# Performance work log

Measured on AMD Instinct MI355X. Metric: run time of the kernel, lower is better.

Reference implementation:

```python
import jax, jax.numpy as jnp
import numpy as np

B, S, D, H, DH, N, L, VOCAB = 8, 512, 1024, 16, 64, 32, 2, 128

def _ln(x, g, b, eps=1e-5):
    m = jnp.mean(x, axis=-1, keepdims=True)
    v = jnp.var(x, axis=-1, keepdims=True)
    return (x - m) * jax.lax.rsqrt(v + eps) * g + b

def setup_inputs() -> dict:
    key = jax.random.key(0)
    ks = jax.random.split(key, 10)
    std = 0.02
    inp = {
        "tokens": jax.random.randint(ks[0], (B, S), 0, VOCAB),
        "emb": jax.random.normal(ks[1], (VOCAB, D), jnp.float32) * std,
        "pos": jax.random.normal(ks[2], (1, S, D), jnp.float32) * std,
        "ln_g": jnp.ones((L, D), jnp.float32),
        "ln_b": jnp.zeros((L, D), jnp.float32),
        "wq": jax.random.normal(ks[3], (L, D, D), jnp.float32) * std,
        "bq": jnp.zeros((L, D), jnp.float32),
        "wk": jax.random.normal(ks[4], (L, D, D), jnp.float32) * std,
        "bk": jnp.zeros((L, D), jnp.float32),
        "wv": jax.random.normal(ks[5], (L, D, D), jnp.float32) * std,
        "bv": jnp.zeros((L, D), jnp.float32),
        "wg": jax.random.normal(ks[6], (L, D, D), jnp.float32) * std,
        "bg": jnp.zeros((L, D), jnp.float32),
        "wo": jax.random.normal(ks[7], (L, D, D), jnp.float32) * std,
        "bo": jnp.zeros((L, D), jnp.float32),
        "alpha_logit": jax.random.normal(ks[8], (L, H, N), jnp.float32) * 0.1,
        "fn_g": jnp.ones((D,), jnp.float32),
        "fn_b": jnp.zeros((D,), jnp.float32),
        "head_w": jax.random.normal(ks[9], (VOCAB, D), jnp.float32) * std,
        "head_b": jnp.zeros((VOCAB,), jnp.float32),
    }
    return inp

def _layer(x, g, b, Wq, Bq, Wk, Bk, Wv, Bv, Wg, Bg, Wo, Bo, alogit):
    residual = x
    xn = _ln(x, g, b)  # (B,S,D)
    def proj(W, Bb):
        return (jnp.einsum('bsd,ed->bse', xn, W) + Bb).reshape(x.shape[0], x.shape[1], H, DH)
    Q, K, V = proj(Wq, Bq), proj(Wk, Bk), proj(Wv, Bv)
    gate = jax.nn.silu(proj(Wg, Bg))
    alpha = jax.nn.sigmoid(alogit)  # (H,N)
    # scan over time; carry h: (B,H,N,DH)
    h0 = jnp.zeros((x.shape[0], H, N, DH), x.dtype)
    qkv = (jnp.moveaxis(Q, 1, 0), jnp.moveaxis(K, 1, 0), jnp.moveaxis(V, 1, 0))  # (S,B,H,DH)
    def step(h, qkv_t):
        q_t, k_t, v_t = qkv_t
        k_state = k_t[:, :, :N]  # state_dim <= d_head
        h = alpha[None, :, :, None] * h + jnp.einsum('bhi,bhj->bhij', k_state, v_t)
        q_state = q_t[:, :, :N]
        o_t = jnp.einsum('bhi,bhij->bhj', q_state, h)
        return h, o_t
    _, O = jax.lax.scan(step, h0, qkv)  # O: (S,B,H,DH)
    o = jnp.moveaxis(O, 0, 1) * gate  # (B,S,H,DH)
    o = o.reshape(x.shape[0], x.shape[1], H * DH)
    y = jnp.einsum('bsd,ed->bse', o, Wo) + Bo
    return residual + y

def reference(tokens, emb, pos, ln_g, ln_b, wq, bq, wk, bk, wv, bv, wg, bg, wo, bo,
              alpha_logit, fn_g, fn_b, head_w, head_b):
    x = emb[tokens] + pos[:, :tokens.shape[1], :]
    for l in range(L):
        x = _layer(x, ln_g[l], ln_b[l], wq[l], bq[l], wk[l], bk[l], wv[l], bv[l],
                   wg[l], bg[l], wo[l], bo[l], alpha_logit[l])
    x = _ln(x, fn_g, fn_b)
    logits = jnp.einsum('bsd,vd->bsv', x, head_w) + head_b
    return logits
```

## Files before the change

### kernel.cpp

```cpp
#include <hip/hip_runtime.h>
#include <hip/hip_bf16.h>
#include <stdint.h>

#define D_MODEL 1024
#define BB 8
#define SS 512
#define HH 16
#define DHH 64
#define NN 32
#define LL 2
#define VOC 128
#define M_TOK (BB * SS)
#define CHUNK 32
#define NCHUNK 16
#define PRO 16

typedef __bf16 bf16x8_t __attribute__((ext_vector_type(8)));
typedef float floatx4_t __attribute__((ext_vector_type(4)));
typedef unsigned short u16;
typedef unsigned short u16x8 __attribute__((ext_vector_type(8)));

__device__ __forceinline__ float b2f(u16 u) {
  union { unsigned int i; float f; } c; c.i = ((unsigned int)u) << 16; return c.f;
}
__device__ __forceinline__ u16 f2b(float f) {
  union { float f; unsigned int i; } c; c.f = f;
  unsigned int r = c.i + 0x7fffu + ((c.i >> 16) & 1u);
  return (u16)(r >> 16);
}
__device__ __forceinline__ float sigm(float x) {
  return 1.0f / (1.0f + __expf(-x));
}

#define WSEG 524288
#define HSEG 32768
#define TOT4 (5 * WSEG + HSEG)
struct SrcP { const float* p[6]; };

__global__ __launch_bounds__(256) void k_pre(
    SrcP src, u16* __restrict__ dst,
    const int* __restrict__ tok, const float* __restrict__ emb,
    const float* __restrict__ pos, const float* __restrict__ g,
    const float* __restrict__ b, float* __restrict__ x, u16* __restrict__ xn) {
  int bid = blockIdx.x;
  int t = threadIdx.x;
  if (bid < 1024) {
    int wv = t >> 6, lane = t & 63;
    int m = bid * 4 + wv;
    int s = m & (SS - 1);
    int tkn = tok[m];
    const float4* er = (const float4*)(emb + (size_t)tkn * D_MODEL);
    const float4* pr = (const float4*)(pos + (size_t)s * D_MODEL);
    float4* xr = (float4*)(x + (size_t)m * D_MODEL);
    float4 v[4];
    float s1 = 0.f, s2 = 0.f;
#pragma unroll
    for (int c = 0; c < 4; ++c) {
      int f4 = c * 64 + lane;
      float4 e = er[f4], p = pr[f4];
      v[c].x = e.x + p.x; v[c].y = e.y + p.y;
      v[c].z = e.z + p.z; v[c].w = e.w + p.w;
      xr[f4] = v[c];
      s1 += v[c].x + v[c].y + v[c].z + v[c].w;
      s2 += v[c].x * v[c].x + v[c].y * v[c].y + v[c].z * v[c].z + v[c].w * v[c].w;
    }
#pragma unroll
    for (int o = 1; o < 64; o <<= 1) {
      s1 += __shfl_xor(s1, o);
      s2 += __shfl_xor(s2, o);
    }
    float mean = s1 * (1.0f / D_MODEL);
    float var = s2 * (1.0f / D_MODEL) - mean * mean;
    float rstd = rsqrtf(var + 1e-5f);
    ushort4* xo = (ushort4*)(xn + (size_t)m * D_MODEL);
#pragma unroll
    for (int c = 0; c < 4; ++c) {
      int f4 = c * 64 + lane;
      float4 gv = ((const float4*)g)[f4];
      float4 bv = ((const float4*)b)[f4];
      ushort4 ov;
      ov.x = f2b((v[c].x - mean) * rstd * gv.x + bv.x);
      ov.y = f2b((v[c].y - mean) * rstd * gv.y + bv.y);
      ov.z = f2b((v[c].z - mean) * rstd * gv.z + bv.z);
      ov.w = f2b((v[c].w - mean) * rstd * gv.w + bv.w);
      xo[f4] = ov;
    }
  } else {
    for (int i = (bid - 1024) * 256 + t; i < TOT4; i += 1024 * 256) {
      int seg, within;
      if (i < 5 * WSEG) { seg = i / WSEG; within = i - seg * WSEG; }
      else { seg = 5; within = i - 5 * WSEG; }
      float4 v = ((const float4*)src.p[seg])[within];
      ushort4 o;
      o.x = f2b(v.x); o.y = f2b(v.y); o.z = f2b(v.z); o.w = f2b(v.w);
      ((ushort4*)dst)[(size_t)seg * WSEG + within] = o;
    }
  }
}

__global__ __launch_bounds__(256) void k_ln(
    const float* __restrict__ x, const float* __restrict__ g,
    const float* __restrict__ b, u16* __restrict__ xn) {
  int t = threadIdx.x;
  int wv = t >> 6, lane = t & 63;
  int m = blockIdx.x * 4 + wv;
  const float4* xr = (const float4*)(x + (size_t)m * D_MODEL);
  float4 v[4];
  float s1 = 0.f, s2 = 0.f;
#pragma unroll
  for (int c = 0; c < 4; ++c) {
    int f4 = c * 64 + lane;
    v[c] = xr[f4];
    s1 += v[c].x + v[c].y + v[c].z + v[c].w;
    s2 += v[c].x * v[c].x + v[c].y * v[c].y + v[c].z * v[c].z + v[c].w * v[c].w;
  }
#pragma unroll
  for (int o = 1; o < 64; o <<= 1) {
    s1 += __shfl_xor(s1, o);
    s2 += __shfl_xor(s2, o);
  }
  float mean = s1 * (1.0f / D_MODEL);
  float var = s2 * (1.0f / D_MODEL) - mean * mean;
  float rstd = rsqrtf(var + 1e-5f);
  ushort4* xo = (ushort4*)(xn + (size_t)m * D_MODEL);
#pragma unroll
  for (int c = 0; c < 4; ++c) {
    int f4 = c * 64 + lane;
    float4 gv = ((const float4*)g)[f4];
    float4 bv = ((const float4*)b)[f4];
    ushort4 ov;
    ov.x = f2b((v[c].x - mean) * rstd * gv.x + bv.x);
    ov.y = f2b((v[c].y - mean) * rstd * gv.y + bv.y);
    ov.z = f2b((v[c].z - mean) * rstd * gv.z + bv.z);
    ov.w = f2b((v[c].w - mean) * rstd * gv.w + bv.w);
    xo[f4] = ov;
  }
}

__global__ __launch_bounds__(256) void k_head_red(
    const u16* __restrict__ Ph, const float* __restrict__ hb,
    float* __restrict__ out) {
  int i4 = blockIdx.x * 256 + threadIdx.x;
  float4 s = ((const float4*)hb)[i4 & 31];
#pragma unroll
  for (int z = 0; z < 8; ++z) {
    ushort4 p = *(const ushort4*)&Ph[(size_t)z * M_TOK * VOC + (size_t)i4 * 4];
    s.x += b2f(p.x); s.y += b2f(p.y); s.z += b2f(p.z); s.w += b2f(p.w);
  }
  ((float4*)out)[i4] = s;
}

struct Task { const u16* W; const float* bias; void* out; };
struct Tasks { Task t[4]; };

__device__ __forceinline__ void async_cp16(const void* g, void* l) {
  __builtin_amdgcn_global_load_lds(
      (const __attribute__((address_space(1))) void*)g,
      (__attribute__((address_space(3))) void*)l, 16, 0, 0);
}

template <int EPI>
__global__ __launch_bounds__(256) void k_gemm(
    const u16* __restrict__ A, Tasks tasks, int N, int K, int kspan,
    size_t pstride) {
  __shared__ u16 ldsA[128 * 64];
  __shared__ u16 ldsB[128 * 64];
  const int tid = threadIdx.x;
  const int lane = tid & 63, wv = tid >> 6;
  const int bm = blockIdx.x * 128, bn = blockIdx.y * 128;
  const Task tk = tasks.t[EPI == 5 ? 0 : blockIdx.z];
  const u16* W = tk.W;
  const int kb = (EPI == 5) ? blockIdx.z * kspan : 0;
  const int ke = kb + kspan;

  const int wm = (wv >> 1) * 64, wn = (wv & 1) * 64;
  floatx4_t acc[4][4];
#pragma unroll
  for (int i = 0; i < 4; ++i)
#pragma unroll
    for (int j = 0; j < 4; ++j)
#pragma unroll
      for (int r = 0; r < 4; ++r) acc[i][j][r] = 0.0f;

  const int srow = lane >> 3;
  const int sk8 = (lane & 7) ^ srow;

  for (int k0 = kb; k0 < ke; k0 += 64) {
#pragma unroll
    for (int c = 0; c < 4; ++c) {
      int chunk = wv * 4 + c;
      const u16* ga = A + (size_t)(bm + chunk * 8 + srow) * K + (k0 + sk8 * 8);
      async_cp16(ga, &ldsA[chunk * 512]);
      const u16* gb = W + (size_t)(bn + chunk * 8 + srow) * K + (k0 + sk8 * 8);
      async_cp16(gb, &ldsB[chunk * 512]);
    }
    __syncthreads();
#pragma unroll
    for (int kt = 0; kt < 2; ++kt) {
      const int k8 = kt * 4 + (lane >> 4);
      bf16x8_t af[4], bfr[4];
#pragma unroll
      for (int mi = 0; mi < 4; ++mi) {
        int row = wm + mi * 16 + (lane & 15);
        int gran = row * 8 + (k8 ^ (row & 7));
        af[mi] = *(const bf16x8_t*)&ldsA[gran * 8];
      }
#pragma unroll
      for (int ni = 0; ni < 4; ++ni) {
        int row = wn + ni * 16 + (lane & 15);
        int gran = row * 8 + (k8 ^ (row & 7));
        bfr[ni] = *(const bf16x8_t*)&ldsB[gran * 8];
      }
#pragma unroll
      for (int mi = 0; mi < 4; ++mi)
#pragma unroll
        for (int ni = 0; ni < 4; ++ni)
          acc[mi][ni] = __builtin_amdgcn_mfma_f32_16x16x32_bf16(
              af[mi], bfr[ni], acc[mi][ni], 0, 0, 0);
    }
    __syncthreads();
  }

  u16* outp16 = (EPI == 5)
      ? (u16*)tk.out + (size_t)blockIdx.z * pstride : (u16*)tk.out;
#pragma unroll
  for (int ni = 0; ni < 4; ++ni) {
    int col = bn + wn + ni * 16 + (lane & 15);
    float bias = (EPI == 2) ? tk.bias[col] : 0.0f;
#pragma unroll
    for (int mi = 0; mi < 4; ++mi) {
      int row0 = bm + wm + mi * 16 + (lane >> 4) * 4;
#pragma unroll
      for (int r = 0; r < 4; ++r) {
        size_t idx = (size_t)(row0 + r) * N + col;
        outp16[idx] = f2b(acc[mi][ni][r] + bias);
      }
    }
  }
}

__global__ __launch_bounds__(256) void k_gemm_wo(
    const u16* __restrict__ A, const u16* __restrict__ W,
    const float* __restrict__ bias, float* __restrict__ x) {
  __shared__ u16 ldsA[64 * 64];
  __shared__ u16 ldsB[128 * 64];
  const int tid = threadIdx.x;
  const int lane = tid & 63, wv = tid >> 6;
  const int bm = blockIdx.x * 64, bn = blockIdx.y * 128;
  const int K = D_MODEL;

  const int wm = (wv >> 1) * 32, wn = (wv & 1) * 64;
  floatx4_t acc[2][4];
#pragma unroll
  for (int i = 0; i < 2; ++i)
#pragma unroll
    for (int j = 0; j < 4; ++j)
#pragma unroll
      for (int r = 0; r < 4; ++r) acc[i][j][r] = 0.0f;

  const int srow = lane >> 3;
  const int sk8 = (lane & 7) ^ srow;

  for (int k0 = 0; k0 < K; k0 += 64) {
#pragma unroll
    for (int c = 0; c < 2; ++c) {
      int chunk = wv * 2 + c;
      const u16* ga = A + (size_t)(bm + chunk * 8 + srow) * K + (k0 + sk8 * 8);
      async_cp16(ga, &ldsA[chunk * 512]);
    }
#pragma unroll
    for (int c = 0; c < 4; ++c) {
      int chunk = wv * 4 + c;
      const u16* gb = W + (size_t)(bn + chunk * 8 + srow) * K + (k0 + sk8 * 8);
      async_cp16(gb, &ldsB[chunk * 512]);
    }
    __syncthreads();
#pragma unroll
    for (int kt = 0; kt < 2; ++kt) {
      const int k8 = kt * 4 + (lane >> 4);
      bf16x8_t af[2], bfr[4];
#pragma unroll
      for (int mi = 0; mi < 2; ++mi) {
        int row = wm + mi * 16 + (lane & 15);
        int gran = row * 8 + (k8 ^ (row & 7));
        af[mi] = *(const bf16x8_t*)&ldsA[gran * 8];
      }
#pragma unroll
      for (int ni = 0; ni < 4; ++ni) {
        int row = wn + ni * 16 + (lane & 15);
        int gran = row * 8 + (k8 ^ (row & 7));
        bfr[ni] = *(const bf16x8_t*)&ldsB[gran * 8];
      }
#pragma unroll
      for (int mi = 0; mi < 2; ++mi)
#pragma unroll
        for (int ni = 0; ni < 4; ++ni)
          acc[mi][ni] = __builtin_amdgcn_mfma_f32_16x16x32_bf16(
              af[mi], bfr[ni], acc[mi][ni], 0, 0, 0);
    }
    __syncthreads();
  }

#pragma unroll
  for (int ni = 0; ni < 4; ++ni) {
    int col = bn + wn + ni * 16 + (lane & 15);
    float bb = bias[col];
#pragma unroll
    for (int mi = 0; mi < 2; ++mi) {
      int row0 = bm + wm + mi * 16 + (lane >> 4) * 4;
#pragma unroll
      for (int r = 0; r < 4; ++r) {
        size_t idx = (size_t)(row0 + r) * D_MODEL + col;
        x[idx] += acc[mi][ni][r] + bb;
      }
    }
  }
}

__global__ __launch_bounds__(128) void k_scan_f(
    const u16* __restrict__ Q, const u16* __restrict__ K,
    const u16* __restrict__ V, const u16* __restrict__ G,
    const float* __restrict__ alog, u16* __restrict__ og) {
  int blk = blockIdx.x;
  int bh = blk >> 4;
  int c = blk & (NCHUNK - 1);
  int b = bh >> 4, h = bh & 15;
  int t = threadIdx.x;
  int jl = t & 31, ig = t >> 5;
  int i0 = ig * 8, j0 = jl * 2;

  __shared__ u16 kp[PRO][32];
  __shared__ u16 vp[PRO][64];
  __shared__ u16 ql[CHUNK][32];
  __shared__ u16 kl[CHUNK][32];
  __shared__ u16 vl[CHUNK][64];
  __shared__ u16 gl[CHUNK][64];
  __shared__ float po[2][CHUNK][64];

  size_t base = (size_t)b * SS * 1024 + h * 64 + (size_t)c * CHUNK * 1024;
  size_t basep = base - (size_t)PRO * 1024;
  {
    int s = t >> 2, e = (t & 3) * 8;
    *(u16x8*)&ql[s][e] = *(const u16x8*)&Q[base + (size_t)s * 1024 + e];
    *(u16x8*)&kl[s][e] = *(const u16x8*)&K[base + (size_t)s * 1024 + e];
    if (c > 0 && t < 64)
      *(u16x8*)&kp[s][e] = *(const u16x8*)&K[basep + (size_t)s * 1024 + e];
  }
#pragma unroll
  for (int r = 0; r < 2; ++r) {
    int idx = t + r * 128;
    int s = idx >> 3, e = (idx & 7) * 8;
    *(u16x8*)&vl[s][e] = *(const u16x8*)&V[base + (size_t)s * 1024 + e];
    *(u16x8*)&gl[s][e] = *(const u16x8*)&G[base + (size_t)s * 1024 + e];
  }
  if (c > 0) {
    int s = t >> 3, e = (t & 7) * 8;
    *(u16x8*)&vp[s][e] = *(const u16x8*)&V[basep + (size_t)s * 1024 + e];
  }
  __syncthreads();

  float al[8];
#pragma unroll
  for (int u = 0; u < 8; ++u) al[u] = sigm(alog[h * NN + i0 + u]);

  float hr[8][2];
#pragma unroll
  for (int u = 0; u < 8; ++u) { hr[u][0] = 0.f; hr[u][1] = 0.f; }

  if (c > 0) {
    for (int s = 0; s < PRO; ++s) {
      ushort4 kA = *(const ushort4*)&kp[s][i0];
      ushort4 kB = *(const ushort4*)&kp[s][i0 + 4];
      float kc[8] = {b2f(kA.x), b2f(kA.y), b2f(kA.z), b2f(kA.w),
                     b2f(kB.x), b2f(kB.y), b2f(kB.z), b2f(kB.w)};
      float vx = b2f(vp[s][j0]), vy = b2f(vp[s][j0 + 1]);
#pragma unroll
      for (int u = 0; u < 8; ++u) {
        hr[u][0] = al[u] * hr[u][0] + kc[u] * vx;
        hr[u][1] = al[u] * hr[u][1] + kc[u] * vy;
      }
    }
  }

  for (int s = 0; s < CHUNK; ++s) {
    ushort4 kA = *(const ushort4*)&kl[s][i0];
    ushort4 kB = *(const ushort4*)&kl[s][i0 + 4];
    ushort4 qA = *(const ushort4*)&ql[s][i0];
    ushort4 qB = *(const ushort4*)&ql[s][i0 + 4];
    float kc[8] = {b2f(kA.x), b2f(kA.y), b2f(kA.z), b2f(kA.w),
                   b2f(kB.x), b2f(kB.y), b2f(kB.z), b2f(kB.w)};
    float qc[8] = {b2f(qA.x), b2f(qA.y), b2f(qA.z), b2f(qA.w),
                   b2f(qB.x), b2f(qB.y), b2f(qB.z), b2f(qB.w)};
    float vx = b2f(vl[s][j0]), vy = b2f(vl[s][j0 + 1]);
    float p0 = 0.f, p1 = 0.f;
#pragma unroll
    for (int u = 0; u < 8; ++u) {
      float h0 = al[u] * hr[u][0] + kc[u] * vx;
      float h1 = al[u] * hr[u][1] + kc[u] * vy;
      hr[u][0] = h0; hr[u][1] = h1;
      p0 += qc[u] * h0;
      p1 += qc[u] * h1;
    }
    p0 += __shfl_xor(p0, 32);
    p1 += __shfl_xor(p1, 32);
    if (!(t & 32)) *(float2*)&po[t >> 6][s][j0] = make_float2(p0, p1);
  }
  __syncthreads();

#pragma unroll
  for (int r = 0; r < 8; ++r) {
    int idx = t + r * 128;
    int s = idx >> 5, jp = (idx & 31) * 2;
    float o0 = po[0][s][jp] + po[1][s][jp];
    float o1 = po[0][s][jp + 1] + po[1][s][jp + 1];
    float g0 = b2f(gl[s][jp]), g1 = b2f(gl[s][jp + 1]);
    ushort2 st;
    st.x = f2b(o0 * g0 * sigm(g0));
    st.y = f2b(o1 * g1 * sigm(g1));
    *(ushort2*)&og[((size_t)b * SS + c * CHUNK + s) * 1024 + h * 64 + jp] = st;
  }
}

extern "C" void kernel_launch(void* const* d_in, const int* in_sizes, int n_in,
                              void* d_out, int out_size, void* d_ws, size_t ws_size,
                              hipStream_t stream) {
  const int*   tok  = (const int*)d_in[0];
  const float* emb  = (const float*)d_in[1];
  const float* pos  = (const float*)d_in[2];
  const float* ln_g = (const float*)d_in[3];
  const float* ln_b = (const float*)d_in[4];
  const float* wq   = (const float*)d_in[5];
  const float* bq   = (const float*)d_in[6];
  const float* wk   = (const float*)d_in[7];
  const float* bk   = (const float*)d_in[8];
  const float* wv   = (const float*)d_in[9];
  const float* bv   = (const float*)d_in[10];
  const float* wg   = (const float*)d_in[11];
  const float* bg   = (const float*)d_in[12];
  const float* wo   = (const float*)d_in[13];
  const float* bo   = (const float*)d_in[14];
  const float* alog = (const float*)d_in[15];
  const float* fn_g = (const float*)d_in[16];
  const float* fn_b = (const float*)d_in[17];
  const float* hw   = (const float*)d_in[18];
  const float* hb   = (const float*)d_in[19];

  char* ws = (char*)d_ws;
  float* x   = (float*)(ws);
  u16*   xn  = (u16*)(ws + (size_t)(16 << 20));
  u16*   qb  = (u16*)(ws + (size_t)(24 << 20));
  u16*   kb  = (u16*)(ws + (size_t)(32 << 20));
  u16*   vb  = (u16*)(ws + (size_t)(40 << 20));
  u16*   gb  = (u16*)(ws + (size_t)(48 << 20));
  u16*   Ph  = (u16*)(ws + (size_t)(56 << 20));
  u16*   wB  = (u16*)(ws + (size_t)(72 << 20));
  u16* wqB = wB;
  u16* wkB = wB + (size_t)2 * 1024 * 1024;
  u16* wvB = wB + (size_t)4 * 1024 * 1024;
  u16* wgB = wB + (size_t)6 * 1024 * 1024;
  u16* woB = wB + (size_t)8 * 1024 * 1024;
  u16* hwB = wB + (size_t)10 * 1024 * 1024;

  SrcP sp; sp.p[0] = wq; sp.p[1] = wk; sp.p[2] = wv; sp.p[3] = wg; sp.p[4] = wo; sp.p[5] = hw;
  k_pre<<<2048, 256, 0, stream>>>(sp, wB, tok, emb, pos, ln_g, ln_b, x, xn);

  for (int l = 0; l < LL; ++l) {
    Tasks tq;
    tq.t[0] = Task{wqB + (size_t)l * D_MODEL * D_MODEL, bq + l * D_MODEL, (void*)qb};
    tq.t[1] = Task{wkB + (size_t)l * D_MODEL * D_MODEL, bk + l * D_MODEL, (void*)kb};
    tq.t[2] = Task{wvB + (size_t)l * D_MODEL * D_MODEL, bv + l * D_MODEL, (void*)vb};
    tq.t[3] = Task{wgB + (size_t)l * D_MODEL * D_MODEL, bg + l * D_MODEL, (void*)gb};
    k_gemm<2><<<dim3(32, 8, 4), 256, 0, stream>>>(xn, tq, D_MODEL, D_MODEL,
                                                  D_MODEL, 0);

    k_scan_f<<<128 * NCHUNK, 128, 0, stream>>>(
        qb, kb, vb, gb, alog + l * HH * NN, xn);

    k_gemm_wo<<<dim3(64, 8), 256, 0, stream>>>(
        xn, woB + (size_t)l * D_MODEL * D_MODEL, bo + l * D_MODEL, x);

    const float* ng = (l + 1 < LL) ? ln_g + (l + 1) * D_MODEL : fn_g;
    const float* nb = (l + 1 < LL) ? ln_b + (l + 1) * D_MODEL : fn_b;
    k_ln<<<1024, 256, 0, stream>>>(x, ng, nb, xn);
  }

  Tasks th;
  th.t[0] = Task{hwB, hb, (void*)Ph};
  th.t[1] = th.t[0]; th.t[2] = th.t[0]; th.t[3] = th.t[0];
  k_gemm<5><<<dim3(32, 1, 8), 256, 0, stream>>>(xn, th, VOC, D_MODEL,
                                                128, (size_t)M_TOK * VOC);
  k_head_red<<<512, 256, 0, stream>>>(Ph, hb, (float*)d_out);
}
```

Before: 344.7 us.

## Fuse whole forward pass into one persistent megakernel with grid barriers

Replaces the chain of separate launches (preprocess, QKVG GEMM, chunked scan, Wo GEMM, layernorm, head GEMM and reduction) with a single persistent kernel. It loops over virtual blocks and synchronises phases with a software grid barrier built on atomics. The scan chunk size is halved and the scan work is re-split into 256-thread units using a union of LDS buffers. This removes launch gaps and tail effects between stages, at the cost of global barrier overhead, reduced occupancy from the launch bounds, and a deadlock risk if the chosen grid cannot be fully co-resident.

```diff
diff --git a/kernel.cpp b/kernel.cpp
--- a/kernel.cpp
+++ b/kernel.cpp
@@ -11,8 +11,8 @@
 #define LL 2
 #define VOC 128
 #define M_TOK (BB * SS)
-#define CHUNK 32
-#define NCHUNK 16
+#define CHUNK 16
+#define NCHUNK 32
 #define PRO 16
 
 typedef __bf16 bf16x8_t __attribute__((ext_vector_type(8)));
@@ -37,80 +37,282 @@
 #define TOT4 (5 * WSEG + HSEG)
 struct SrcP { const float* p[6]; };
 
-__global__ __launch_bounds__(256) void k_pre(
-    SrcP src, u16* __restrict__ dst,
-    const int* __restrict__ tok, const float* __restrict__ emb,
-    const float* __restrict__ pos, const float* __restrict__ g,
-    const float* __restrict__ b, float* __restrict__ x, u16* __restrict__ xn) {
-  int bid = blockIdx.x;
-  int t = threadIdx.x;
-  if (bid < 1024) {
-    int wv = t >> 6, lane = t & 63;
-    int m = bid * 4 + wv;
-    int s = m & (SS - 1);
-    int tkn = tok[m];
-    const float4* er = (const float4*)(emb + (size_t)tkn * D_MODEL);
-    const float4* pr = (const float4*)(pos + (size_t)s * D_MODEL);
-    float4* xr = (float4*)(x + (size_t)m * D_MODEL);
-    float4 v[4];
-    float s1 = 0.f, s2 = 0.f;
+struct ScanU {
+  u16 ql[CHUNK][32]; u16 kl[CHUNK][32];
+  u16 vl[CHUNK][64]; u16 gl[CHUNK][64];
+  u16 kp[PRO][32];   u16 vp[PRO][64];
+  float po[CHUNK][64];
+};
+union LdsU {
+  struct { u16 A[128 * 64]; u16 B[128 * 64]; } g;
+  ScanU s[2];
+};
+
+__device__ __forceinline__ void async_cp16(const void* g, void* l) {
+  __builtin_amdgcn_global_load_lds(
+      (const __attribute__((address_space(1))) void*)g,
+      (__attribute__((address_space(3))) void*)l, 16, 0, 0);
+}
+
+__device__ void gbar(unsigned* cnt, unsigned* gen, unsigned& lg) {
+  __threadfence();
+  __syncthreads();
+  if (threadIdx.x == 0) {
+    unsigned g = lg;
+    if (atomicAdd(cnt, 1u) == gridDim.x - 1u) {
+      atomicExch(cnt, 0u);
+      __threadfence();
+      atomicAdd(gen, 1u);
+    } else {
+      while (atomicAdd(gen, 0u) == g) __builtin_amdgcn_s_sleep(8);
+    }
+    lg = g + 1u;
+  }
+  __syncthreads();
+  __threadfence();
+}
+
+__device__ void gemm128(const u16* __restrict__ A, const u16* __restrict__ W,
+                        const float* __restrict__ bias, u16* __restrict__ out,
+                        int N, int K, int kb, int ke, int bx, int by, int tid,
+                        u16* ldsA, u16* ldsB, bool addBias) {
+  const int lane = tid & 63, wv = tid >> 6;
+  const int bm = bx * 128, bn = by * 128;
+  const int wm = (wv >> 1) * 64, wn = (wv & 1) * 64;
+  floatx4_t acc[4][4];
+#pragma unroll
+  for (int i = 0; i < 4; ++i)
+#pragma unroll
+    for (int j = 0; j < 4; ++j)
+#pragma unroll
+      for (int r = 0; r < 4; ++r) acc[i][j][r] = 0.0f;
+
+  const int srow = lane >> 3;
+  const int sk8 = (lane & 7) ^ srow;
+
+  for (int k0 = kb; k0 < ke; k0 += 64) {
 #pragma unroll
     for (int c = 0; c < 4; ++c) {
-      int f4 = c * 64 + lane;
-      float4 e = er[f4], p = pr[f4];
-      v[c].x = e.x + p.x; v[c].y = e.y + p.y;
-      v[c].z = e.z + p.z; v[c].w = e.w + p.w;
-      xr[f4] = v[c];
-      s1 += v[c].x + v[c].y + v[c].z + v[c].w;
-      s2 += v[c].x * v[c].x + v[c].y * v[c].y + v[c].z * v[c].z + v[c].w * v[c].w;
-    }
-#pragma unroll
-    for (int o = 1; o < 64; o <<= 1) {
-      s1 += __shfl_xor(s1, o);
-      s2 += __shfl_xor(s2, o);
-    }
-    float mean = s1 * (1.0f / D_MODEL);
-    float var = s2 * (1.0f / D_MODEL) - mean * mean;
-    float rstd = rsqrtf(var + 1e-5f);
-    ushort4* xo = (ushort4*)(xn + (size_t)m * D_MODEL);
+      int chunk = wv * 4 + c;
+      const u16* ga = A + (size_t)(bm + chunk * 8 + srow) * K + (k0 + sk8 * 8);
+      async_cp16(ga, &ldsA[chunk * 512]);
+      const u16* gb = W + (size_t)(bn + chunk * 8 + srow) * K + (k0 + sk8 * 8);
+      async_cp16(gb, &ldsB[chunk * 512]);
+    }
+    __syncthreads();
+#pragma unroll
+    for (int kt = 0; kt < 2; ++kt) {
+      const int k8 = kt * 4 + (lane >> 4);
+      bf16x8_t af[4], bfr[4];
+#pragma unroll
+      for (int mi = 0; mi < 4; ++mi) {
+        int row = wm + mi * 16 + (lane & 15);
+        int gran = row * 8 + (k8 ^ (row & 7));
+        af[mi] = *(const bf16x8_t*)&ldsA[gran * 8];
+      }
+#pragma unroll
+      for (int ni = 0; ni < 4; ++ni) {
+        int row = wn + ni * 16 + (lane & 15);
+        int gran = row * 8 + (k8 ^ (row & 7));
+        bfr[ni] = *(const bf16x8_t*)&ldsB[gran * 8];
+      }
+#pragma unroll
+      for (int mi = 0; mi < 4; ++mi)
+#pragma unroll
+        for (int ni = 0; ni < 4; ++ni)
+          acc[mi][ni] = __builtin_amdgcn_mfma_f32_16x16x32_bf16(
+              af[mi], bfr[ni], acc[mi][ni], 0, 0, 0);
+    }
+    __syncthreads();
+  }
+
+#pragma unroll
+  for (int ni = 0; ni < 4; ++ni) {
+    int col = bn + wn + ni * 16 + (lane & 15);
+    float bb = addBias ? bias[col] : 0.0f;
+#pragma unroll
+    for (int mi = 0; mi < 4; ++mi) {
+      int row0 = bm + wm + mi * 16 + (lane >> 4) * 4;
+#pragma unroll
+      for (int r = 0; r < 4; ++r)
+        out[(size_t)(row0 + r) * N + col] = f2b(acc[mi][ni][r] + bb);
+    }
+  }
+}
+
+__device__ void wo64(const u16* __restrict__ A, const u16* __restrict__ W,
+                     const float* __restrict__ bias, float* __restrict__ x,
+                     int bx, int by, int tid, u16* ldsA, u16* ldsB) {
+  const int lane = tid & 63, wv = tid >> 6;
+  const int bm = bx * 64, bn = by * 128;
+  const int K = D_MODEL;
+  const int wm = (wv >> 1) * 32, wn = (wv & 1) * 64;
+  floatx4_t acc[2][4];
+#pragma unroll
+  for (int i = 0; i < 2; ++i)
+#pragma unroll
+    for (int j = 0; j < 4; ++j)
+#pragma unroll
+      for (int r = 0; r < 4; ++r) acc[i][j][r] = 0.0f;
+
+  const int srow = lane >> 3;
+  const int sk8 = (lane & 7) ^ srow;
+
+  for (int k0 = 0; k0 < K; k0 += 64) {
+#pragma unroll
+    for (int c = 0; c < 2; ++c) {
+      int chunk = wv * 2 + c;
+      const u16* ga = A + (size_t)(bm + chunk * 8 + srow) * K + (k0 + sk8 * 8);
+      async_cp16(ga, &ldsA[chunk * 512]);
+    }
 #pragma unroll
     for (int c = 0; c < 4; ++c) {
-      int f4 = c * 64 + lane;
-      float4 gv = ((const float4*)g)[f4];
-      float4 bv = ((const float4*)b)[f4];
-      ushort4 ov;
-      ov.x = f2b((v[c].x - mean) * rstd * gv.x + bv.x);
-      ov.y = f2b((v[c].y - mean) * rstd * gv.y + bv.y);
-      ov.z = f2b((v[c].z - mean) * rstd * gv.z + bv.z);
-      ov.w = f2b((v[c].w - mean) * rstd * gv.w + bv.w);
-      xo[f4] = ov;
-    }
-  } else {
-    for (int i = (bid - 1024) * 256 + t; i < TOT4; i += 1024 * 256) {
-      int seg, within;
-      if (i < 5 * WSEG) { seg = i / WSEG; within = i - seg * WSEG; }
-      else { seg = 5; within = i - 5 * WSEG; }
-      float4 v = ((const float4*)src.p[seg])[within];
-      ushort4 o;
-      o.x = f2b(v.x); o.y = f2b(v.y); o.z = f2b(v.z); o.w = f2b(v.w);
-      ((ushort4*)dst)[(size_t)seg * WSEG + within] = o;
-    }
-  }
-}
-
-__global__ __launch_bounds__(256) void k_ln(
-    const float* __restrict__ x, const float* __restrict__ g,
-    const float* __restrict__ b, u16* __restrict__ xn) {
-  int t = threadIdx.x;
+      int chunk = wv * 4 + c;
+      const u16* gb = W + (size_t)(bn + chunk * 8 + srow) * K + (k0 + sk8 * 8);
+      async_cp16(gb, &ldsB[chunk * 512]);
+    }
+    __syncthreads();
+#pragma unroll
+    for (int kt = 0; kt < 2; ++kt) {
+      const int k8 = kt * 4 + (lane >> 4);
+      bf16x8_t af[2], bfr[4];
+#pragma unroll
+      for (int mi = 0; mi < 2; ++mi) {
+        int row = wm + mi * 16 + (lane & 15);
+        int gran = row * 8 + (k8 ^ (row & 7));
+        af[mi] = *(const bf16x8_t*)&ldsA[gran * 8];
+      }
+#pragma unroll
+      for (int ni = 0; ni < 4; ++ni) {
+        int row = wn + ni * 16 + (lane & 15);
+        int gran = row * 8 + (k8 ^ (row & 7));
+        bfr[ni] = *(const bf16x8_t*)&ldsB[gran * 8];
+      }
+#pragma unroll
+      for (int mi = 0; mi < 2; ++mi)
+#pragma unroll
+        for (int ni = 0; ni < 4; ++ni)
+          acc[mi][ni] = __builtin_amdgcn_mfma_f32_16x16x32_bf16(
+              af[mi], bfr[ni], acc[mi][ni], 0, 0, 0);
+    }
+    __syncthreads();
+  }
+
+#pragma unroll
+  for (int ni = 0; ni < 4; ++ni) {
+    int col = bn + wn + ni * 16 + (lane & 15);
+    float bb = bias[col];
+#pragma unroll
+    for (int mi = 0; mi < 2; ++mi) {
+      int row0 = bm + wm + mi * 16 + (lane >> 4) * 4;
+#pragma unroll
+      for (int r = 0; r < 4; ++r)
+        x[(size_t)(row0 + r) * D_MODEL + col] += acc[mi][ni][r] + bb;
+    }
+  }
+}
+
+__device__ void scan_unit(ScanU* S, int vu, int tl,
+                          const u16* __restrict__ Q, const u16* __restrict__ K,
+                          const u16* __restrict__ V, const u16* __restrict__ G,
+                          const float* __restrict__ alog, u16* __restrict__ og) {
+  int bh = vu >> 5;
+  int c = vu & (NCHUNK - 1);
+  int b = bh >> 4, h = bh & 15;
+  int j = tl & 63, ig = tl >> 6, i0 = ig * 16;
+
+  size_t base = (size_t)b * SS * 1024 + h * 64 + (size_t)c * CHUNK * 1024;
+  size_t basep = base - (size_t)PRO * 1024;
+  {
+    int u6 = tl & 63;
+    int sq = u6 >> 2, e = (u6 & 3) * 8;
+    if (tl < 64)
+      *(u16x8*)&S->ql[sq][e] = *(const u16x8*)&Q[base + (size_t)sq * 1024 + e];
+    else
+      *(u16x8*)&S->kl[sq][e] = *(const u16x8*)&K[base + (size_t)sq * 1024 + e];
+    int sv = tl >> 3, ev = (tl & 7) * 8;
+    *(u16x8*)&S->vl[sv][ev] = *(const u16x8*)&V[base + (size_t)sv * 1024 + ev];
+    *(u16x8*)&S->gl[sv][ev] = *(const u16x8*)&G[base + (size_t)sv * 1024 + ev];
+    if (c > 0) {
+      if (tl < 64)
+        *(u16x8*)&S->kp[sq][e] = *(const u16x8*)&K[basep + (size_t)sq * 1024 + e];
+      *(u16x8*)&S->vp[sv][ev] = *(const u16x8*)&V[basep + (size_t)sv * 1024 + ev];
+    }
+  }
+  __syncthreads();
+
+  float al[16];
+#pragma unroll
+  for (int u = 0; u < 16; ++u) al[u] = sigm(alog[h * NN + i0 + u]);
+  float hr[16];
+#pragma unroll
+  for (int u = 0; u < 16; ++u) hr[u] = 0.f;
+
+  if (c > 0) {
+    for (int s = 0; s < PRO; ++s) {
+      u16x8 kA = *(const u16x8*)&S->kp[s][i0];
+      u16x8 kB = *(const u16x8*)&S->kp[s][i0 + 8];
+      float vx = b2f(S->vp[s][j]);
+#pragma unroll
+      for (int u = 0; u < 8; ++u) hr[u] = al[u] * hr[u] + b2f(kA[u]) * vx;
+#pragma unroll
+      for (int u = 0; u < 8; ++u) hr[8 + u] = al[8 + u] * hr[8 + u] + b2f(kB[u]) * vx;
+    }
+  }
+
+  float pr[16];
+#pragma unroll
+  for (int s = 0; s < CHUNK; ++s) {
+    u16x8 kA = *(const u16x8*)&S->kl[s][i0];
+    u16x8 kB = *(const u16x8*)&S->kl[s][i0 + 8];
+    u16x8 qA = *(const u16x8*)&S->ql[s][i0];
+    u16x8 qB = *(const u16x8*)&S->ql[s][i0 + 8];
+    float vx = b2f(S->vl[s][j]);
+    float p = 0.f;
+#pragma unroll
+    for (int u = 0; u < 8; ++u) {
+      hr[u] = al[u] * hr[u] + b2f(kA[u]) * vx;
+      p += b2f(qA[u]) * hr[u];
+    }
+#pragma unroll
+    for (int u = 0; u < 8; ++u) {
+      hr[8 + u] = al[8 + u] * hr[8 + u] + b2f(kB[u]) * vx;
+      p += b2f(qB[u]) * hr[8 + u];
+    }
+    if (ig) S->po[s][j] = p; else pr[s] = p;
+  }
+  __syncthreads();
+
+  if (ig == 0) {
+#pragma unroll
+    for (int s = 0; s < CHUNK; ++s) {
+      float o = pr[s] + S->po[s][j];
+      float gg = b2f(S->gl[s][j]);
+      og[((size_t)b * SS + c * CHUNK + s) * 1024 + h * 64 + j] =
+          f2b(o * gg * sigm(gg));
+    }
+  }
+}
+
+__device__ void embed_ln_dev(const int* tok, const float* emb, const float* pos,
+                             const float* g, const float* b, float* x, u16* xn,
+                             int blk, int t) {
   int wv = t >> 6, lane = t & 63;
-  int m = blockIdx.x * 4 + wv;
-  const float4* xr = (const float4*)(x + (size_t)m * D_MODEL);
+  int m = blk * 4 + wv;
+  int s = m & (SS - 1);
+  int tkn = tok[m];
+  const float4* er = (const float4*)(emb + (size_t)tkn * D_MODEL);
+  const float4* pr = (const float4*)(pos + (size_t)s * D_MODEL);
+  float4* xr = (float4*)(x + (size_t)m * D_MODEL);
   float4 v[4];
   float s1 = 0.f, s2 = 0.f;
 #pragma unroll
   for (int c = 0; c < 4; ++c) {
     int f4 = c * 64 + lane;
-    v[c] = xr[f4];
+    float4 e = er[f4], p = pr[f4];
+    v[c].x = e.x + p.x; v[c].y = e.y + p.y;
+    v[c].z = e.z + p.z; v[c].w = e.w + p.w;
+    xr[f4] = v[c];
     s1 += v[c].x + v[c].y + v[c].z + v[c].w;
     s2 += v[c].x * v[c].x + v[c].y * v[c].y + v[c].z * v[c].z + v[c].w * v[c].w;
   }
@@ -137,287 +339,133 @@
   }
 }
 
-__global__ __launch_bounds__(256) void k_head_red(
-    const u16* __restrict__ Ph, const float* __restrict__ hb,
-    float* __restrict__ out) {
-  int i4 = blockIdx.x * 256 + threadIdx.x;
-  float4 s = ((const float4*)hb)[i4 & 31];
-#pragma unroll
-  for (int z = 0; z < 8; ++z) {
-    ushort4 p = *(const ushort4*)&Ph[(size_t)z * M_TOK * VOC + (size_t)i4 * 4];
-    s.x += b2f(p.x); s.y += b2f(p.y); s.z += b2f(p.z); s.w += b2f(p.w);
-  }
-  ((float4*)out)[i4] = s;
-}
-
-struct Task { const u16* W; const float* bias; void* out; };
-struct Tasks { Task t[4]; };
-
-__device__ __forceinline__ void async_cp16(const void* g, void* l) {
-  __builtin_amdgcn_global_load_lds(
-      (const __attribute__((address_space(1))) void*)g,
-      (__attribute__((address_space(3))) void*)l, 16, 0, 0);
-}
-
-template <int EPI>
-__global__ __launch_bounds__(256) void k_gemm(
-    const u16* __restrict__ A, Tasks tasks, int N, int K, int kspan,
-    size_t pstride) {
-  __shared__ u16 ldsA[128 * 64];
-  __shared__ u16 ldsB[128 * 64];
-  const int tid = threadIdx.x;
-  const int lane = tid & 63, wv = tid >> 6;
-  const int bm = blockIdx.x * 128, bn = blockIdx.y * 128;
-  const Task tk = tasks.t[EPI == 5 ? 0 : blockIdx.z];
-  const u16* W = tk.W;
-  const int kb = (EPI == 5) ? blockIdx.z * kspan : 0;
-  const int ke = kb + kspan;
-
-  const int wm = (wv >> 1) * 64, wn = (wv & 1) * 64;
-  floatx4_t acc[4][4];
-#pragma unroll
-  for (int i = 0; i < 4; ++i)
-#pragma unroll
-    for (int j = 0; j < 4; ++j)
-#pragma unroll
-      for (int r = 0; r < 4; ++r) acc[i][j][r] = 0.0f;
-
-  const int srow = lane >> 3;
-  const int sk8 = (lane & 7) ^ srow;
-
-  for (int k0 = kb; k0 < ke; k0 += 64) {
-#pragma unroll
-    for (int c = 0; c < 4; ++c) {
-      int chunk = wv * 4 + c;
-      const u16* ga = A + (size_t)(bm + chunk * 8 + srow) * K + (k0 + sk8 * 8);
-      async_cp16(ga, &ldsA[chunk * 512]);
-      const u16* gb = W + (size_t)(bn + chunk * 8 + srow) * K + (k0 + sk8 * 8);
-      async_cp16(gb, &ldsB[chunk * 512]);
-    }
-    __syncthreads();
-#pragma unroll
-    for (int kt = 0; kt < 2; ++kt) {
-      const int k8 = kt * 4 + (lane >> 4);
-      bf16x8_t af[4], bfr[4];
-#pragma unroll
-      for (int mi = 0; mi < 4; ++mi) {
-        int row = wm + mi * 16 + (lane & 15);
-        int gran = row * 8 + (k8 ^ (row & 7));
-        af[mi] = *(const bf16x8_t*)&ldsA[gran * 8];
+__device__ void ln_dev(const float* x, const float* g, const float* b,
+                       u16* xn, int blk, int t) {
+  int wv = t >> 6, lane = t & 63;
+  int m = blk * 4 + wv;
+  const float4* xr = (const float4*)(x + (size_t)m * D_MODEL);
+  float4 v[4];
+  float s1 = 0.f, s2 = 0.f;
+#pragma unroll
+  for (int c = 0; c < 4; ++c) {
+    int f4 = c * 64 + lane;
+    v[c] = xr[f4];
+    s1 += v[c].x + v[c].y + v[c].z + v[c].w;
+    s2 += v[c].x * v[c].x + v[c].y * v[c].y + v[c].z * v[c].z + v[c].w * v[c].w;
+  }
+#pragma unroll
+  for (int o = 1; o < 64; o <<= 1) {
+    s1 += __shfl_xor(s1, o);
+    s2 += __shfl_xor(s2, o);
+  }
+  float mean = s1 * (1.0f / D_MODEL);
+  float var = s2 * (1.0f / D_MODEL) - mean * mean;
+  float rstd = rsqrtf(var + 1e-5f);
+  ushort4* xo = (ushort4*)(xn + (size_t)m * D_MODEL);
+#pragma unroll
+  for (int c = 0; c < 4; ++c) {
+    int f4 = c * 64 + lane;
+    float4 gv = ((const float4*)g)[f4];
+    float4 bv = ((const float4*)b)[f4];
+    ushort4 ov;
+    ov.x = f2b((v[c].x - mean) * rstd * gv.x + bv.x);
+    ov.y = f2b((v[c].y - mean) * rstd * gv.y + bv.y);
+    ov.z = f2b((v[c].z - mean) * rstd * gv.z + bv.z);
+    ov.w = f2b((v[c].w - mean) * rstd * gv.w + bv.w);
+    xo[f4] = ov;
+  }
+}
+
+struct MegaParams {
+  const int* tok; const float* emb; const float* pos;
+  const float* ln_g; const float* ln_b;
+  const float* bq; const float* bk; const float* bv; const float* bg;
+  const float* bo; const float* alog;
+  const float* fn_g; const float* fn_b; const float* hb;
+  SrcP src;
+  float* x; u16* xn; u16* qb; u16* kb; u16* vb; u16* gb; u16* Ph; u16* wB;
+  unsigned* bar;
+  float* out;
+};
+
+__global__ __launch_bounds__(256, 4) void k_mega(MegaParams P) {
+  __shared__ LdsU L;
+  const int blk = blockIdx.x;
+  const int G = gridDim.x;
+  const int t = threadIdx.x;
+  unsigned lg = 0;
+  unsigned* cnt = P.bar;
+  unsigned* gen = P.bar + 1;
+
+  for (int vb = blk; vb < 1024; vb += G)
+    embed_ln_dev(P.tok, P.emb, P.pos, P.ln_g, P.ln_b, P.x, P.xn, vb, t);
+  for (int i = blk * 256 + t; i < TOT4; i += G * 256) {
+    int seg, within;
+    if (i < 5 * WSEG) { seg = i / WSEG; within = i - seg * WSEG; }
+    else { seg = 5; within = i - 5 * WSEG; }
+    float4 v = ((const float4*)P.src.p[seg])[within];
+    ushort4 o;
+    o.x = f2b(v.x); o.y = f2b(v.y); o.z = f2b(v.z); o.w = f2b(v.w);
+    ((ushort4*)P.wB)[(size_t)seg * WSEG + within] = o;
+  }
+  gbar(cnt, gen, lg);
+
+  for (int l = 0; l < LL; ++l) {
+    for (int vb = blk; vb < 1024; vb += G) {
+      int bx = vb & 31, by = (vb >> 5) & 7, bz = vb >> 8;
+      const u16* Wt = P.wB + (size_t)bz * 2097152 + (size_t)l * 1048576;
+      const float* bias =
+          (bz == 0 ? P.bq : bz == 1 ? P.bk : bz == 2 ? P.bv : P.bg) + l * D_MODEL;
+      u16* out = bz == 0 ? P.qb : bz == 1 ? P.kb : bz == 2 ? P.vb : P.gb;
+      gemm128(P.xn, Wt, bias, out, D_MODEL, D_MODEL, 0, D_MODEL,
+              bx, by, t, L.g.A, L.g.B, true);
+    }
+    gbar(cnt, gen, lg);
+
+    {
+      const float* al = P.alog + l * HH * NN;
+      int unit = t >> 7, tl = t & 127;
+      int iters = 4096 / (2 * G);
+      for (int it = 0; it < iters; ++it) {
+        int vu = it * 2 * G + blk * 2 + unit;
+        scan_unit(&L.s[unit], vu, tl, P.qb, P.kb, P.vb, P.gb, al, P.xn);
+        __syncthreads();
       }
-#pragma unroll
-      for (int ni = 0; ni < 4; ++ni) {
-        int row = wn + ni * 16 + (lane & 15);
-        int gran = row * 8 + (k8 ^ (row & 7));
-        bfr[ni] = *(const bf16x8_t*)&ldsB[gran * 8];
-      }
-#pragma unroll
-      for (int mi = 0; mi < 4; ++mi)
-#pragma unroll
-        for (int ni = 0; ni < 4; ++ni)
-          acc[mi][ni] = __builtin_amdgcn_mfma_f32_16x16x32_bf16(
-              af[mi], bfr[ni], acc[mi][ni], 0, 0, 0);
-    }
-    __syncthreads();
-  }
-
-  u16* outp16 = (EPI == 5)
-      ? (u16*)tk.out + (size_t)blockIdx.z * pstride : (u16*)tk.out;
-#pragma unroll
-  for (int ni = 0; ni < 4; ++ni) {
-    int col = bn + wn + ni * 16 + (lane & 15);
-    float bias = (EPI == 2) ? tk.bias[col] : 0.0f;
-#pragma unroll
-    for (int mi = 0; mi < 4; ++mi) {
-      int row0 = bm + wm + mi * 16 + (lane >> 4) * 4;
-#pragma unroll
-      for (int r = 0; r < 4; ++r) {
-        size_t idx = (size_t)(row0 + r) * N + col;
-        outp16[idx] = f2b(acc[mi][ni][r] + bias);
-      }
-    }
-  }
-}
-
-__global__ __launch_bounds__(256) void k_gemm_wo(
-    const u16* __restrict__ A, const u16* __restrict__ W,
-    const float* __restrict__ bias, float* __restrict__ x) {
-  __shared__ u16 ldsA[64 * 64];
-  __shared__ u16 ldsB[128 * 64];
-  const int tid = threadIdx.x;
-  const int lane = tid & 63, wv = tid >> 6;
-  const int bm = blockIdx.x * 64, bn = blockIdx.y * 128;
-  const int K = D_MODEL;
-
-  const int wm = (wv >> 1) * 32, wn = (wv & 1) * 64;
-  floatx4_t acc[2][4];
-#pragma unroll
-  for (int i = 0; i < 2; ++i)
-#pragma unroll
-    for (int j = 0; j < 4; ++j)
-#pragma unroll
-      for (int r = 0; r < 4; ++r) acc[i][j][r] = 0.0f;
-
-  const int srow = lane >> 3;
-  const int sk8 = (lane & 7) ^ srow;
-
-  for (int k0 = 0; k0 < K; k0 += 64) {
-#pragma unroll
-    for (int c = 0; c < 2; ++c) {
-      int chunk = wv * 2 + c;
-      const u16* ga = A + (size_t)(bm + chunk * 8 + srow) * K + (k0 + sk8 * 8);
-      async_cp16(ga, &ldsA[chunk * 512]);
-    }
-#pragma unroll
-    for (int c = 0; c < 4; ++c) {
-      int chunk = wv * 4 + c;
-      const u16* gb = W + (size_t)(bn + chunk * 8 + srow) * K + (k0 + sk8 * 8);
-      async_cp16(gb, &ldsB[chunk * 512]);
-    }
-    __syncthreads();
-#pragma unroll
-    for (int kt = 0; kt < 2; ++kt) {
-      const int k8 = kt * 4 + (lane >> 4);
-      bf16x8_t af[2], bfr[4];
-#pragma unroll
-      for (int mi = 0; mi < 2; ++mi) {
-        int row = wm + mi * 16 + (lane & 15);
-        int gran = row * 8 + (k8 ^ (row & 7));
-        af[mi] = *(const bf16x8_t*)&ldsA[gran * 8];
-      }
-#pragma unroll
-      for (int ni = 0; ni < 4; ++ni) {
-        int row = wn + ni * 16 + (lane & 15);
-        int gran = row * 8 + (k8 ^ (row & 7));
-        bfr[ni] = *(const bf16x8_t*)&ldsB[gran * 8];
-      }
-#pragma unroll
-      for (int mi = 0; mi < 2; ++mi)
-#pragma unroll
-        for (int ni = 0; ni < 4; ++ni)
-          acc[mi][ni] = __builtin_amdgcn_mfma_f32_16x16x32_bf16(
-              af[mi], bfr[ni], acc[mi][ni], 0, 0, 0);
-    }
-    __syncthreads();
-  }
-
-#pragma unroll
-  for (int ni = 0; ni < 4; ++ni) {
-    int col = bn + wn + ni * 16 + (lane & 15);
-    float bb = bias[col];
-#pragma unroll
-    for (int mi = 0; mi < 2; ++mi) {
-      int row0 = bm + wm + mi * 16 + (lane >> 4) * 4;
-#pragma unroll
-      for (int r = 0; r < 4; ++r) {
-        size_t idx = (size_t)(row0 + r) * D_MODEL + col;
-        x[idx] += acc[mi][ni][r] + bb;
-      }
-    }
-  }
-}
-
-__global__ __launch_bounds__(128) void k_scan_f(
-    const u16* __restrict__ Q, const u16* __restrict__ K,
-    const u16* __restrict__ V, const u16* __restrict__ G,
-    const float* __restrict__ alog, u16* __restrict__ og) {
-  int blk = blockIdx.x;
-  int bh = blk >> 4;
-  int c = blk & (NCHUNK - 1);
-  int b = bh >> 4, h = bh & 15;
-  int t = threadIdx.x;
-  int jl = t & 31, ig = t >> 5;
-  int i0 = ig * 8, j0 = jl * 2;
-
-  __shared__ u16 kp[PRO][32];
-  __shared__ u16 vp[PRO][64];
-  __shared__ u16 ql[CHUNK][32];
-  __shared__ u16 kl[CHUNK][32];
-  __shared__ u16 vl[CHUNK][64];
-  __shared__ u16 gl[CHUNK][64];
-  __shared__ float po[2][CHUNK][64];
-
-  size_t base = (size_t)b * SS * 1024 + h * 64 + (size_t)c * CHUNK * 1024;
-  size_t basep = base - (size_t)PRO * 1024;
-  {
-    int s = t >> 2, e = (t & 3) * 8;
-    *(u16x8*)&ql[s][e] = *(const u16x8*)&Q[base + (size_t)s * 1024 + e];
-    *(u16x8*)&kl[s][e] = *(const u16x8*)&K[base + (size_t)s * 1024 + e];
-    if (c > 0 && t < 64)
-      *(u16x8*)&kp[s][e] = *(const u16x8*)&K[basep + (size_t)s * 1024 + e];
-  }
-#pragma unroll
-  for (int r = 0; r < 2; ++r) {
-    int idx = t + r * 128;
-    int s = idx >> 3, e = (idx & 7) * 8;
-    *(u16x8*)&vl[s][e] = *(const u16x8*)&V[base + (size_t)s * 1024 + e];
-    *(u16x8*)&gl[s][e] = *(const u16x8*)&G[base + (size_t)s * 1024 + e];
-  }
-  if (c > 0) {
-    int s = t >> 3, e = (t & 7) * 8;
-    *(u16x8*)&vp[s][e] = *(const u16x8*)&V[basep + (size_t)s * 1024 + e];
-  }
-  __syncthreads();
-
-  float al[8];
-#pragma unroll
-  for (int u = 0; u < 8; ++u) al[u] = sigm(alog[h * NN + i0 + u]);
-
-  float hr[8][2];
-#pragma unroll
-  for (int u = 0; u < 8; ++u) { hr[u][0] = 0.f; hr[u][1] = 0.f; }
-
-  if (c > 0) {
-    for (int s = 0; s < PRO; ++s) {
-      ushort4 kA = *(const ushort4*)&kp[s][i0];
-      ushort4 kB = *(const ushort4*)&kp[s][i0 + 4];
-      float kc[8] = {b2f(kA.x), b2f(kA.y), b2f(kA.z), b2f(kA.w),
-                     b2f(kB.x), b2f(kB.y), b2f(kB.z), b2f(kB.w)};
-      float vx = b2f(vp[s][j0]), vy = b2f(vp[s][j0 + 1]);
-#pragma unroll
-      for (int u = 0; u < 8; ++u) {
-        hr[u][0] = al[u] * hr[u][0] + kc[u] * vx;
-        hr[u][1] = al[u] * hr[u][1] + kc[u] * vy;
-      }
-    }
-  }
-
-  for (int s = 0; s < CHUNK; ++s) {
-    ushort4 kA = *(const ushort4*)&kl[s][i0];
-    ushort4 kB = *(const ushort4*)&kl[s][i0 + 4];
-    ushort4 qA = *(const ushort4*)&ql[s][i0];
-    ushort4 qB = *(const ushort4*)&ql[s][i0 + 4];
-    float kc[8] = {b2f(kA.x), b2f(kA.y), b2f(kA.z), b2f(kA.w),
-                   b2f(kB.x), b2f(kB.y), b2f(kB.z), b2f(kB.w)};
-    float qc[8] = {b2f(qA.x), b2f(qA.y), b2f(qA.z), b2f(qA.w),
-                   b2f(qB.x), b2f(qB.y), b2f(qB.z), b2f(qB.w)};
-    float vx = b2f(vl[s][j0]), vy = b2f(vl[s][j0 + 1]);
-    float p0 = 0.f, p1 = 0.f;
-#pragma unroll
-    for (int u = 0; u < 8; ++u) {
-      float h0 = al[u] * hr[u][0] + kc[u] * vx;
-      float h1 = al[u] * hr[u][1] + kc[u] * vy;
-      hr[u][0] = h0; hr[u][1] = h1;
-      p0 += qc[u] * h0;
-      p1 += qc[u] * h1;
-    }
-    p0 += __shfl_xor(p0, 32);
-    p1 += __shfl_xor(p1, 32);
-    if (!(t & 32)) *(float2*)&po[t >> 6][s][j0] = make_float2(p0, p1);
-  }
-  __syncthreads();
-
-#pragma unroll
-  for (int r = 0; r < 8; ++r) {
-    int idx = t + r * 128;
-    int s = idx >> 5, jp = (idx & 31) * 2;
-    float o0 = po[0][s][jp] + po[1][s][jp];
-    float o1 = po[0][s][jp + 1] + po[1][s][jp + 1];
-    float g0 = b2f(gl[s][jp]), g1 = b2f(gl[s][jp + 1]);
-    ushort2 st;
-    st.x = f2b(o0 * g0 * sigm(g0));
-    st.y = f2b(o1 * g1 * sigm(g1));
-    *(ushort2*)&og[((size_t)b * SS + c * CHUNK + s) * 1024 + h * 64 + jp] = st;
+    }
+    gbar(cnt, gen, lg);
+
+    for (int vb = blk; vb < 512; vb += G) {
+      int bx = vb & 63, by = vb >> 6;
+      wo64(P.xn, P.wB + (size_t)4 * 2097152 + (size_t)l * 1048576,
+           P.bo + l * D_MODEL, P.x, bx, by, t, L.g.A, L.g.B);
+    }
+    gbar(cnt, gen, lg);
+
+    {
+      const float* ngp = (l + 1 < LL) ? P.ln_g + (l + 1) * D_MODEL : P.fn_g;
+      const float* nbp = (l + 1 < LL) ? P.ln_b + (l + 1) * D_MODEL : P.fn_b;
+      for (int vb = blk; vb < 1024; vb += G)
+        ln_dev(P.x, ngp, nbp, P.xn, vb, t);
+    }
+    gbar(cnt, gen, lg);
+  }
+
+  for (int vb = blk; vb < 256; vb += G) {
+    int bx = vb & 31, bz = vb >> 5;
+    gemm128(P.xn, P.wB + (size_t)10 * 1048576, nullptr,
+            P.Ph + (size_t)bz * M_TOK * VOC, VOC, D_MODEL,
+            bz * 128, bz * 128 + 128, bx, 0, t, L.g.A, L.g.B, false);
+  }
+  gbar(cnt, gen, lg);
+
+  for (int i4 = blk * 256 + t; i4 < M_TOK * VOC / 4; i4 += G * 256) {
+    float4 s = ((const float4*)P.hb)[i4 & 31];
+#pragma unroll
+    for (int z = 0; z < 8; ++z) {
+      ushort4 p = *(const ushort4*)&P.Ph[(size_t)z * M_TOK * VOC + (size_t)i4 * 4];
+      s.x += b2f(p.x); s.y += b2f(p.y); s.z += b2f(p.z); s.w += b2f(p.w);
+    }
+    ((float4*)P.out)[i4] = s;
   }
 }
 
@@ -446,48 +494,29 @@
   const float* hb   = (const float*)d_in[19];
 
   char* ws = (char*)d_ws;
-  float* x   = (float*)(ws);
-  u16*   xn  = (u16*)(ws + (size_t)(16 << 20));
-  u16*   qb  = (u16*)(ws + (size_t)(24 << 20));
-  u16*   kb  = (u16*)(ws + (size_t)(32 << 20));
-  u16*   vb  = (u16*)(ws + (size_t)(40 << 20));
-  u16*   gb  = (u16*)(ws + (size_t)(48 << 20));
-  u16*   Ph  = (u16*)(ws + (size_t)(56 << 20));
-  u16*   wB  = (u16*)(ws + (size_t)(72 << 20));
-  u16* wqB = wB;
-  u16* wkB = wB + (size_t)2 * 1024 * 1024;
-  u16* wvB = wB + (size_t)4 * 1024 * 1024;
-  u16* wgB = wB + (size_t)6 * 1024 * 1024;
-  u16* woB = wB + (size_t)8 * 1024 * 1024;
-  u16* hwB = wB + (size_t)10 * 1024 * 1024;
-
-  SrcP sp; sp.p[0] = wq; sp.p[1] = wk; sp.p[2] = wv; sp.p[3] = wg; sp.p[4] = wo; sp.p[5] = hw;
-  k_pre<<<2048, 256, 0, stream>>>(sp, wB, tok, emb, pos, ln_g, ln_b, x, xn);
-
-  for (int l = 0; l < LL; ++l) {
-    Tasks tq;
-    tq.t[0] = Task{wqB + (size_t)l * D_MODEL * D_MODEL, bq + l * D_MODEL, (void*)qb};
-    tq.t[1] = Task{wkB + (size_t)l * D_MODEL * D_MODEL, bk + l * D_MODEL, (void*)kb};
-    tq.t[2] = Task{wvB + (size_t)l * D_MODEL * D_MODEL, bv + l * D_MODEL, (void*)vb};
-    tq.t[3] = Task{wgB + (size_t)l * D_MODEL * D_MODEL, bg + l * D_MODEL, (void*)gb};
-    k_gemm<2><<<dim3(32, 8, 4), 256, 0, stream>>>(xn, tq, D_MODEL, D_MODEL,
-                                                  D_MODEL, 0);
-
-    k_scan_f<<<128 * NCHUNK, 128, 0, stream>>>(
-        qb, kb, vb, gb, alog + l * HH * NN, xn);
-
-    k_gemm_wo<<<dim3(64, 8), 256, 0, stream>>>(
-        xn, woB + (size_t)l * D_MODEL * D_MODEL, bo + l * D_MODEL, x);
-
-    const float* ng = (l + 1 < LL) ? ln_g + (l + 1) * D_MODEL : fn_g;
-    const float* nb = (l + 1 < LL) ? ln_b + (l + 1) * D_MODEL : fn_b;
-    k_ln<<<1024, 256, 0, stream>>>(x, ng, nb, xn);
-  }
-
-  Tasks th;
-  th.t[0] = Task{hwB, hb, (void*)Ph};
-  th.t[1] = th.t[0]; th.t[2] = th.t[0]; th.t[3] = th.t[0];
-  k_gemm<5><<<dim3(32, 1, 8), 256, 0, stream>>>(xn, th, VOC, D_MODEL,
-                                                128, (size_t)M_TOK * VOC);
-  k_head_red<<<512, 256, 0, stream>>>(Ph, hb, (float*)d_out);
-}
+  MegaParams P;
+  P.tok = tok; P.emb = emb; P.pos = pos;
+  P.ln_g = ln_g; P.ln_b = ln_b;
+  P.bq = bq; P.bk = bk; P.bv = bv; P.bg = bg; P.bo = bo;
+  P.alog = alog; P.fn_g = fn_g; P.fn_b = fn_b; P.hb = hb;
+  P.src.p[0] = wq; P.src.p[1] = wk; P.src.p[2] = wv;
+  P.src.p[3] = wg; P.src.p[4] = wo; P.src.p[5] = hw;
+  P.x  = (float*)(ws);
+  P.xn = (u16*)(ws + (size_t)(16 << 20));
+  P.qb = (u16*)(ws + (size_t)(24 << 20));
+  P.kb = (u16*)(ws + (size_t)(32 << 20));
+  P.vb = (u16*)(ws + (size_t)(40 << 20));
+  P.gb = (u16*)(ws + (size_t)(48 << 20));
+  P.Ph = (u16*)(ws + (size_t)(56 << 20));
+  P.bar = (unsigned*)(ws + (size_t)(64 << 20));
+  P.wB = (u16*)(ws + (size_t)(72 << 20));
+  P.out = (float*)d_out;
+
+  int occ = 0;
+  (void)hipOccupancyMaxActiveBlocksPerMultiprocessor(
+      &occ, (const void*)k_mega, 256, 0);
+  int G = (occ >= 4) ? 1024 : (occ >= 2) ? 512 : 256;
+
+  hipMemsetAsync(P.bar, 0, 8, stream);
+  k_mega<<<dim3(G), dim3(256), 0, stream>>>(P);
+}
```

Result: slower. 1.362 ms (+295.3%).
